# Kernel optimization log

Hardware: AMD Instinct MI355X
Metric: run time of the kernel (lower is better)

Reference implementation:

```python
import jax, jax.numpy as jnp
import numpy as np

NUM_NODES = 100000
EMBED_DIM = 128
COMP_DIM = 64
T = 8
NSUB = 50000


def layer_norm(x, g, b, eps=1e-5):
    mu = jnp.mean(x, axis=-1, keepdims=True)
    var = jnp.mean((x - mu) ** 2, axis=-1, keepdims=True)
    return (x - mu) * jax.lax.rsqrt(var + eps) * g + b


def setup_inputs() -> dict:
    key = jax.random.key(0)
    ks = jax.random.split(key, 12)
    D, C = EMBED_DIM, COMP_DIM
    s = lambda n: 1.0 / np.sqrt(n)
    return {
        "x": jax.random.normal(ks[0], (T * NSUB, D), dtype=jnp.float32),
        "indices": jax.random.randint(ks[1], (T, NSUB), 0, NUM_NODES, dtype=jnp.int64),
        "bd": jax.random.normal(ks[2], (NUM_NODES, D), dtype=jnp.float32),
        "ln_d_g": jnp.ones((D,), jnp.float32), "ln_d_b": jnp.zeros((D,), jnp.float32),
        "Wd1": jax.random.normal(ks[3], (D, 2 * D), jnp.float32) * s(D),
        "bd1": jnp.zeros((2 * D,), jnp.float32),
        "Wd2": jax.random.normal(ks[4], (2 * D, C), jnp.float32) * s(2 * D),
        "bd2": jnp.zeros((C,), jnp.float32),
        "ln_u_g": jnp.ones((C,), jnp.float32), "ln_u_b": jnp.zeros((C,), jnp.float32),
        "Wu1": jax.random.normal(ks[5], (C, 2 * C), jnp.float32) * s(C),
        "bu1": jnp.zeros((2 * C,), jnp.float32),
        "Wu2": jax.random.normal(ks[6], (2 * C, D), jnp.float32) * s(2 * C),
        "bu2": jnp.zeros((D,), jnp.float32),
    }


def reference(x, indices, bd, ln_d_g, ln_d_b, Wd1, bd1, Wd2, bd2,
              ln_u_g, ln_u_b, Wu1, bu1, Wu2, bu2):
    # _to_entire: per-timestep scatter-add of subnode feats into full node table
    x3 = x.reshape(T, NSUB, EMBED_DIM)  # [T, Nsub, D]
    scattered = jax.vmap(
        lambda xt, it: jax.ops.segment_sum(xt, it, num_segments=NUM_NODES)
    )(x3, indices)  # [T, num_nodes, D]
    inp = scattered + bd[None]  # ta + bd (use_bd=True)
    h = layer_norm(inp, ln_d_g, ln_d_b)
    # mlp_d: Linear -> GELU -> Dropout(eval=identity) -> Linear
    h = jax.nn.gelu(h @ Wd1 + bd1, approximate=False) @ Wd2 + bd2  # [T, num_nodes, C]
    # _from_entire: gather activated rows per timestep, then LN + mlp_u
    gathered = jax.vmap(lambda ht, it: ht[it])(h, indices)  # [T, Nsub, C]
    g = gathered.reshape(T * NSUB, COMP_DIM)
    u = layer_norm(g, ln_u_g, ln_u_b)
    out = jax.nn.gelu(u @ Wu1 + bu1, approximate=False) @ Wu2 + bu2  # [T*Nsub, D]
    return out
```

## Files before the change

### kernel.cpp

```cpp
#include <hip/hip_runtime.h>
#include <math.h>

#define NN 100000
#define DD 128
#define CC 64
#define TT 8
#define NS 50000
#define G8 8
#define MAXS2 196
#define BCAP 16

typedef __attribute__((ext_vector_type(4))) float f32x4;
typedef __attribute__((ext_vector_type(8))) short bf16x8;

__device__ __forceinline__ short f2bf(float f) {
    union { float f; unsigned u; } v; v.f = f;
    unsigned r = v.u + 0x7fffu + ((v.u >> 16) & 1u);
    return (short)(r >> 16);
}
__device__ __forceinline__ float gelu(float x) {
    float t = x + 0.044715f * x * x * x;
    return x / (1.0f + __expf(-1.5957691216f * t));
}

__global__ void prep_all(const float* __restrict__ Wd1, const float* __restrict__ Wd2,
                         const float* __restrict__ Wu1, const float* __restrict__ Wu2,
                         short* __restrict__ pW1, short* __restrict__ pW2,
                         short* __restrict__ pW3, short* __restrict__ pW4) {
    int b = blockIdx.x;
    const float* W; short* dst; int KSTEPS, total, N, s0;
    if (b < 16)      { W = Wd1; dst = pW1; KSTEPS = 4; total = 4096; N = 256; s0 = b * 256; }
    else if (b < 24) { W = Wd2; dst = pW2; KSTEPS = 8; total = 2048; N = 64;  s0 = (b - 16) * 256; }
    else if (b < 28) { W = Wu1; dst = pW3; KSTEPS = 2; total = 1024; N = 128; s0 = (b - 24) * 256; }
    else             { W = Wu2; dst = pW4; KSTEPS = 4; total = 2048; N = 128; s0 = (b - 28) * 256; }
    int s = s0 + threadIdx.x;
    if (s >= total) return;
    int lane = s & 63;
    int ks = (s >> 6) % KSTEPS;
    int n = s / (64 * KSTEPS);
    int kb = ks * 32 + (lane >> 4) * 8;
    int col = n * 16 + (lane & 15);
    bf16x8 o;
    #pragma unroll
    for (int j = 0; j < 8; ++j) o[j] = f2bf(W[(size_t)(kb + j) * N + col]);
    *(bf16x8*)(dst + (size_t)s * 8) = o;
}

__global__ void flagfill_kernel(const int* __restrict__ idx, int* __restrict__ pernode,
                                int* __restrict__ bucket) {
    int i = blockIdx.x * 256 + threadIdx.x;
    if (i >= G8 * NS) return;
    int g = i / NS, s = i - g * NS;
    int node = idx[i];
    int p = atomicAdd(&pernode[node * 8 + g], 1);
    if (p < BCAP) bucket[((size_t)node * 8 + g) * BCAP + p] = s;
}

__global__ void compact_kernel(const int* __restrict__ pernode,
                               int* __restrict__ lists, int* __restrict__ cnts) {
    int g = blockIdx.y;
    int node = blockIdx.x * 256 + threadIdx.x;
    bool active = (node < NN) && (pernode[node * 8 + g] > 0);
    unsigned long long m = __ballot(active);
    int lane = threadIdx.x & 63;
    int rank = __popcll(m & ((1ull << lane) - 1ull));
    int nact = __popcll(m);
    int lbase = 0;
    if (lane == 0 && nact > 0) lbase = atomicAdd(&cnts[g], nact);
    lbase = __shfl(lbase, 0);
    if (active) lists[(size_t)g * NS + lbase + rank] = node;
}

__global__ __launch_bounds__(1024, 4) void fused_kernel(
    const float* __restrict__ x, const float* __restrict__ bd,
    const float* __restrict__ lndg, const float* __restrict__ lndb,
    const short* __restrict__ pW1, const short* __restrict__ pW2,
    const short* __restrict__ pW3, const short* __restrict__ pW4,
    const float* __restrict__ bd1, const float* __restrict__ bd2,
    const float* __restrict__ lnug, const float* __restrict__ lnub,
    const float* __restrict__ bu1, const float* __restrict__ bu2,
    const int* __restrict__ lists, const int* __restrict__ cnts,
    const int* __restrict__ pernode, const int* __restrict__ bucket,
    float* __restrict__ out) {
    __shared__ short sW1[4096 * 8];
    __shared__ short sW2[2048 * 8];
    __shared__ short sW4[2048 * 8];
    __shared__ short sBuf[16][1024];

    const int tid = threadIdx.x;
    for (int s = tid; s < 4096; s += 1024)
        *(bf16x8*)(sW1 + s * 8) = *(const bf16x8*)(pW1 + (size_t)s * 8);
    for (int s = tid; s < 2048; s += 1024)
        *(bf16x8*)(sW2 + s * 8) = *(const bf16x8*)(pW2 + (size_t)s * 8);
    for (int s = tid; s < 2048; s += 1024)
        *(bf16x8*)(sW4 + s * 8) = *(const bf16x8*)(pW4 + (size_t)s * 8);
    __syncthreads();

    const int wave = tid >> 6, lane = tid & 63;
    short* myb = sBuf[wave];
    const int arow = lane & 15;
    const int kgrp = lane >> 4;

    for (int w = blockIdx.x; w < G8 * MAXS2; w += gridDim.x) {
        const int g = w % G8;
        const int strip = w / G8;
        const int nrows = cnts[g];
        if (strip * 256 >= nrows) continue;
        const int* list = lists + (size_t)g * NS;
        const float* x_g = x + (size_t)g * NS * DD;
        float* out_g = out + (size_t)g * NS * DD;
        const int row0 = strip * 256 + wave * 16;

        const int gi = row0 + arow;
        const int node = list[gi < nrows ? gi : nrows - 1];
        const int c = pernode[node * 8 + g];
        const size_t bbase = ((size_t)node * 8 + g) * BCAP;
        const int4 p4 = *(const int4*)(bucket + bbase);
        float v[32];
        {
            const float* bp = bd + (size_t)node * DD + kgrp * 8;
            #pragma unroll
            for (int ks = 0; ks < 4; ++ks) {
                float4 b0 = *(const float4*)(bp + ks * 32);
                float4 b1 = *(const float4*)(bp + ks * 32 + 4);
                v[ks*8+0]=b0.x; v[ks*8+1]=b0.y; v[ks*8+2]=b0.z; v[ks*8+3]=b0.w;
                v[ks*8+4]=b1.x; v[ks*8+5]=b1.y; v[ks*8+6]=b1.z; v[ks*8+7]=b1.w;
            }
        }
        {
            const int i1 = (c > 1) ? p4.y : p4.x;
            const float m1 = (c > 1) ? 1.f : 0.f;
            const float* xp0 = x_g + (size_t)p4.x * DD + kgrp * 8;
            const float* xp1 = x_g + (size_t)i1 * DD + kgrp * 8;
            float4 A0[8], A1[8];
            #pragma unroll
            for (int q = 0; q < 8; ++q) A0[q] = *(const float4*)(xp0 + (q >> 1) * 32 + (q & 1) * 4);
            #pragma unroll
            for (int q = 0; q < 8; ++q) A1[q] = *(const float4*)(xp1 + (q >> 1) * 32 + (q & 1) * 4);
            #pragma unroll
            for (int q = 0; q < 8; ++q) {
                v[q*4+0] += A0[q].x; v[q*4+1] += A0[q].y; v[q*4+2] += A0[q].z; v[q*4+3] += A0[q].w;
                v[q*4+0] = fmaf(m1, A1[q].x, v[q*4+0]);
                v[q*4+1] = fmaf(m1, A1[q].y, v[q*4+1]);
                v[q*4+2] = fmaf(m1, A1[q].z, v[q*4+2]);
                v[q*4+3] = fmaf(m1, A1[q].w, v[q*4+3]);
            }
            if (__any(c > 2)) {
                const int i2 = (c > 2) ? p4.z : p4.x;
                const int i3 = (c > 3) ? p4.w : p4.x;
                const float m2 = (c > 2) ? 1.f : 0.f;
                const float m3 = (c > 3) ? 1.f : 0.f;
                const float* xp2 = x_g + (size_t)i2 * DD + kgrp * 8;
                const float* xp3 = x_g + (size_t)i3 * DD + kgrp * 8;
                #pragma unroll
                for (int q = 0; q < 8; ++q) A0[q] = *(const float4*)(xp2 + (q >> 1) * 32 + (q & 1) * 4);
                #pragma unroll
                for (int q = 0; q < 8; ++q) A1[q] = *(const float4*)(xp3 + (q >> 1) * 32 + (q & 1) * 4);
                #pragma unroll
                for (int q = 0; q < 8; ++q) {
                    v[q*4+0] = fmaf(m2, A0[q].x, v[q*4+0]);
                    v[q*4+1] = fmaf(m2, A0[q].y, v[q*4+1]);
                    v[q*4+2] = fmaf(m2, A0[q].z, v[q*4+2]);
                    v[q*4+3] = fmaf(m2, A0[q].w, v[q*4+3]);
                    v[q*4+0] = fmaf(m3, A1[q].x, v[q*4+0]);
                    v[q*4+1] = fmaf(m3, A1[q].y, v[q*4+1]);
                    v[q*4+2] = fmaf(m3, A1[q].z, v[q*4+2]);
                    v[q*4+3] = fmaf(m3, A1[q].w, v[q*4+3]);
                }
                int j = 4;
                while (__any(j < c) && j < BCAP) {
                    const int pj = (j < c) ? bucket[bbase + j] : p4.x;
                    const float mj = (j < c) ? 1.f : 0.f;
                    const float* xpj = x_g + (size_t)pj * DD + kgrp * 8;
                    #pragma unroll
                    for (int q = 0; q < 8; ++q) A0[q] = *(const float4*)(xpj + (q >> 1) * 32 + (q & 1) * 4);
                    #pragma unroll
                    for (int q = 0; q < 8; ++q) {
                        v[q*4+0] = fmaf(mj, A0[q].x, v[q*4+0]);
                        v[q*4+1] = fmaf(mj, A0[q].y, v[q*4+1]);
                        v[q*4+2] = fmaf(mj, A0[q].z, v[q*4+2]);
                        v[q*4+3] = fmaf(mj, A0[q].w, v[q*4+3]);
                    }
                    ++j;
                }
            }
        }
        float s1 = 0.f;
        #pragma unroll
        for (int j = 0; j < 32; ++j) s1 += v[j];
        s1 += __shfl_xor(s1, 16); s1 += __shfl_xor(s1, 32);
        float mu = s1 * 0.0078125f;
        float s2 = 0.f;
        #pragma unroll
        for (int j = 0; j < 32; ++j) { float d = v[j] - mu; s2 += d * d; }
        s2 += __shfl_xor(s2, 16); s2 += __shfl_xor(s2, 32);
        float rs = rsqrtf(s2 * 0.0078125f + 1e-5f);
        bf16x8 afr[4];
        {
            const float* gp = lndg + kgrp * 8;
            const float* bbp = lndb + kgrp * 8;
            #pragma unroll
            for (int ks = 0; ks < 4; ++ks) {
                float4 g0 = *(const float4*)(gp + ks * 32);
                float4 g1 = *(const float4*)(gp + ks * 32 + 4);
                float4 c0 = *(const float4*)(bbp + ks * 32);
                float4 c1 = *(const float4*)(bbp + ks * 32 + 4);
                afr[ks][0] = f2bf((v[ks*8+0]-mu)*rs*g0.x + c0.x);
                afr[ks][1] = f2bf((v[ks*8+1]-mu)*rs*g0.y + c0.y);
                afr[ks][2] = f2bf((v[ks*8+2]-mu)*rs*g0.z + c0.z);
                afr[ks][3] = f2bf((v[ks*8+3]-mu)*rs*g0.w + c0.w);
                afr[ks][4] = f2bf((v[ks*8+4]-mu)*rs*g1.x + c1.x);
                afr[ks][5] = f2bf((v[ks*8+5]-mu)*rs*g1.y + c1.y);
                afr[ks][6] = f2bf((v[ks*8+6]-mu)*rs*g1.z + c1.z);
                afr[ks][7] = f2bf((v[ks*8+7]-mu)*rs*g1.w + c1.w);
            }
        }
        f32x4 acc2[4];
        #pragma unroll
        for (int n = 0; n < 4; ++n) acc2[n] = (f32x4){0.f, 0.f, 0.f, 0.f};
        for (int ks2 = 0; ks2 < 8; ++ks2) {
            f32x4 a1[2];
            a1[0] = (f32x4){0.f, 0.f, 0.f, 0.f};
            a1[1] = (f32x4){0.f, 0.f, 0.f, 0.f};
            #pragma unroll
            for (int ks1 = 0; ks1 < 4; ++ks1) {
                #pragma unroll
                for (int p = 0; p < 2; ++p) {
                    bf16x8 bf = *(const bf16x8*)(sW1 + (size_t)((((2*ks2+p) << 2) | ks1) * 64 + lane) * 8);
                    a1[p] = __builtin_amdgcn_mfma_f32_16x16x32_bf16(afr[ks1], bf, a1[p], 0, 0, 0);
                }
            }
            #pragma unroll
            for (int p = 0; p < 2; ++p) {
                float bias = bd1[(2*ks2+p) * 16 + arow];
                #pragma unroll
                for (int rr = 0; rr < 4; ++rr) {
                    float vv = gelu(a1[p][rr] + bias);
                    int row = kgrp * 4 + rr;
                    int byte = row * 64 + (((p * 16 + arow) * 2) ^ ((row & 3) << 4));
                    myb[byte >> 1] = f2bf(vv);
                }
            }
            bf16x8 af2 = *(const bf16x8*)(myb + ((arow * 64 + ((kgrp * 16) ^ ((arow & 3) << 4))) >> 1));
            #pragma unroll
            for (int n2 = 0; n2 < 4; ++n2) {
                bf16x8 bf = *(const bf16x8*)(sW2 + (size_t)(((n2 << 3) | ks2) * 64 + lane) * 8);
                acc2[n2] = __builtin_amdgcn_mfma_f32_16x16x32_bf16(af2, bf, acc2[n2], 0, 0, 0);
            }
        }
        float hv[4][4];
        #pragma unroll
        for (int n2 = 0; n2 < 4; ++n2)
            #pragma unroll
            for (int rr = 0; rr < 4; ++rr)
                hv[n2][rr] = acc2[n2][rr] + bd2[n2 * 16 + arow];
        float mu_u[4], rs_u[4];
        #pragma unroll
        for (int rr = 0; rr < 4; ++rr) {
            float sr = hv[0][rr] + hv[1][rr] + hv[2][rr] + hv[3][rr];
            sr += __shfl_xor(sr, 1); sr += __shfl_xor(sr, 2);
            sr += __shfl_xor(sr, 4); sr += __shfl_xor(sr, 8);
            mu_u[rr] = sr * 0.015625f;
            float sq = 0.f;
            #pragma unroll
            for (int n2 = 0; n2 < 4; ++n2) { float d = hv[n2][rr] - mu_u[rr]; sq += d * d; }
            sq += __shfl_xor(sq, 1); sq += __shfl_xor(sq, 2);
            sq += __shfl_xor(sq, 4); sq += __shfl_xor(sq, 8);
            rs_u[rr] = rsqrtf(sq * 0.015625f + 1e-5f);
        }
        #pragma unroll
        for (int n2 = 0; n2 < 4; ++n2) {
            int cidx = n2 * 16 + arow;
            float gg = lnug[cidx], bb = lnub[cidx];
            #pragma unroll
            for (int rr = 0; rr < 4; ++rr) {
                float nv = (hv[n2][rr] - mu_u[rr]) * rs_u[rr] * gg + bb;
                int row = kgrp * 4 + rr;
                int byte = row * 128 + ((cidx * 2) ^ ((row & 7) << 4));
                myb[byte >> 1] = f2bf(nv);
            }
        }
        bf16x8 af3[2];
        #pragma unroll
        for (int ks3 = 0; ks3 < 2; ++ks3)
            af3[ks3] = *(const bf16x8*)(myb + ((arow * 128 + ((ks3 * 64 + kgrp * 16) ^ ((arow & 7) << 4))) >> 1));
        f32x4 acc4[8];
        #pragma unroll
        for (int n = 0; n < 8; ++n) acc4[n] = (f32x4){0.f, 0.f, 0.f, 0.f};
        #pragma unroll
        for (int half = 0; half < 2; ++half) {
            f32x4 a3[4];
            #pragma unroll
            for (int n = 0; n < 4; ++n) a3[n] = (f32x4){0.f, 0.f, 0.f, 0.f};
            #pragma unroll
            for (int ks3 = 0; ks3 < 2; ++ks3) {
                #pragma unroll
                for (int n3h = 0; n3h < 4; ++n3h) {
                    int n3 = half * 4 + n3h;
                    bf16x8 bf = *(const bf16x8*)(pW3 + (size_t)(((n3 << 1) | ks3) * 64 + lane) * 8);
                    a3[n3h] = __builtin_amdgcn_mfma_f32_16x16x32_bf16(af3[ks3], bf, a3[n3h], 0, 0, 0);
                }
            }
            #pragma unroll
            for (int n3h = 0; n3h < 4; ++n3h) {
                float bias = bu1[(half * 4 + n3h) * 16 + arow];
                #pragma unroll
                for (int rr = 0; rr < 4; ++rr) {
                    float vv = gelu(a3[n3h][rr] + bias);
                    int row = kgrp * 4 + rr;
                    int byte = row * 128 + (((n3h * 16 + arow) * 2) ^ ((row & 7) << 4));
                    myb[byte >> 1] = f2bf(vv);
                }
            }
            #pragma unroll
            for (int k4 = 0; k4 < 2; ++k4) {
                bf16x8 afu = *(const bf16x8*)(myb + ((arow * 128 + ((k4 * 64 + kgrp * 16) ^ ((arow & 7) << 4))) >> 1));
                #pragma unroll
                for (int n4 = 0; n4 < 8; ++n4) {
                    bf16x8 bf = *(const bf16x8*)(sW4 + (size_t)(((n4 << 2) | (half * 2 + k4)) * 64 + lane) * 8);
                    acc4[n4] = __builtin_amdgcn_mfma_f32_16x16x32_bf16(afu, bf, acc4[n4], 0, 0, 0);
                }
            }
        }
        #pragma unroll
        for (int rr = 0; rr < 4; ++rr) {
            int gi2 = row0 + kgrp * 4 + rr;
            if (gi2 >= nrows) continue;
            int nd = list[gi2];
            int c2 = pernode[nd * 8 + g];
            const size_t bb2 = ((size_t)nd * 8 + g) * BCAP;
            const int4 q4 = *(const int4*)(bucket + bb2);
            float vals[8];
            #pragma unroll
            for (int n4 = 0; n4 < 8; ++n4) vals[n4] = acc4[n4][rr] + bu2[n4 * 16 + arow];
            {
                float* op = out_g + (size_t)q4.x * DD + arow;
                #pragma unroll
                for (int n4 = 0; n4 < 8; ++n4) op[n4 * 16] = vals[n4];
            }
            if (1 < c2) {
                float* op = out_g + (size_t)q4.y * DD + arow;
                #pragma unroll
                for (int n4 = 0; n4 < 8; ++n4) op[n4 * 16] = vals[n4];
            }
            if (2 < c2) {
                float* op = out_g + (size_t)q4.z * DD + arow;
                #pragma unroll
                for (int n4 = 0; n4 < 8; ++n4) op[n4 * 16] = vals[n4];
            }
            if (3 < c2) {
                float* op = out_g + (size_t)q4.w * DD + arow;
                #pragma unroll
                for (int n4 = 0; n4 < 8; ++n4) op[n4 * 16] = vals[n4];
            }
            int j = 4;
            while (__any(j < c2) && j < BCAP) {
                if (j < c2) {
                    int s = bucket[bb2 + j];
                    float* op = out_g + (size_t)s * DD + arow;
                    #pragma unroll
                    for (int n4 = 0; n4 < 8; ++n4) op[n4 * 16] = vals[n4];
                }
                ++j;
            }
        }
    }
}

extern "C" void kernel_launch(void* const* d_in, const int* in_sizes, int n_in,
                              void* d_out, int out_size, void* d_ws, size_t ws_size,
                              hipStream_t stream) {
    const float* x       = (const float*)d_in[0];
    const int*   indices = (const int*)d_in[1];
    const float* bd      = (const float*)d_in[2];
    const float* ln_d_g  = (const float*)d_in[3];
    const float* ln_d_b  = (const float*)d_in[4];
    const float* Wd1     = (const float*)d_in[5];
    const float* bd1     = (const float*)d_in[6];
    const float* Wd2     = (const float*)d_in[7];
    const float* bd2     = (const float*)d_in[8];
    const float* ln_u_g  = (const float*)d_in[9];
    const float* ln_u_b  = (const float*)d_in[10];
    const float* Wu1     = (const float*)d_in[11];
    const float* bu1     = (const float*)d_in[12];
    const float* Wu2     = (const float*)d_in[13];
    const float* bu2     = (const float*)d_in[14];
    float* out = (float*)d_out;

    char* ws = (char*)d_ws;
    size_t o = 0;
    auto alloc_b = [&](size_t bytes) { char* p = ws + o; o = (o + bytes + 255) & ~(size_t)255; return p; };
    int*   pernode  = (int*)alloc_b((size_t)NN * 8 * 4);
    int*   cnts     = (int*)alloc_b(8 * 4);
    size_t zero_bytes = (size_t)((char*)cnts - (char*)pernode) + 256;
    int*   bucket   = (int*)alloc_b((size_t)NN * 8 * BCAP * 4);
    int*   lists    = (int*)alloc_b((size_t)8 * NS * 4);
    short* pW1      = (short*)alloc_b((size_t)4096 * 16);
    short* pW2      = (short*)alloc_b((size_t)2048 * 16);
    short* pW3      = (short*)alloc_b((size_t)1024 * 16);
    short* pW4      = (short*)alloc_b((size_t)2048 * 16);

    hipMemsetAsync(pernode, 0, zero_bytes, stream);

    prep_all<<<36, 256, 0, stream>>>(Wd1, Wd2, Wu1, Wu2, pW1, pW2, pW3, pW4);
    flagfill_kernel<<<(G8 * NS + 255) / 256, 256, 0, stream>>>(indices, pernode, bucket);
    compact_kernel<<<dim3((NN + 255) / 256, G8), 256, 0, stream>>>(pernode, lists, cnts);
    fused_kernel<<<256, 1024, 0, stream>>>(x, bd, ln_d_g, ln_d_b, pW1, pW2, pW3, pW4,
                                           bd1, bd2, ln_u_g, ln_u_b, bu1, bu2,
                                           lists, cnts, pernode, bucket, out);
}
```

Baseline: 468.1 us.

## Prefetch next strip's node metadata and pack bucket indices as 16-bit

Bucket slot indices are stored as 16-bit values, which halves the bucket table footprint and lets a single int4 load return eight source indices instead of four. The fused loop now software-pipelines the list, count and bucket loads for the next work item while the current MLP runs. The aggregation is unrolled up to eight sources with masked FMAs, and LayerNorm outputs are packed to bf16 with the hardware v_cvt_pk_bf16_f32 instruction. The memset now also zeroes the lists region, and the prefetch uses extra registers, which may reduce occupancy.

```diff
diff --git a/kernel.cpp b/kernel.cpp
--- a/kernel.cpp
+++ b/kernel.cpp
@@ -8,15 +8,21 @@
 #define NS 50000
 #define G8 8
 #define MAXS2 196
-#define BCAP 16
+#define TOTW (G8 * MAXS2)
 
 typedef __attribute__((ext_vector_type(4))) float f32x4;
 typedef __attribute__((ext_vector_type(8))) short bf16x8;
+typedef unsigned short ushort_t;
 
 __device__ __forceinline__ short f2bf(float f) {
     union { float f; unsigned u; } v; v.f = f;
     unsigned r = v.u + 0x7fffu + ((v.u >> 16) & 1u);
     return (short)(r >> 16);
+}
+__device__ __forceinline__ unsigned pk_bf16(float lo, float hi) {
+    unsigned r;
+    asm("v_cvt_pk_bf16_f32 %0, %1, %2" : "=v"(r) : "v"(lo), "v"(hi));
+    return r;
 }
 __device__ __forceinline__ float gelu(float x) {
     float t = x + 0.044715f * x * x * x;
@@ -47,13 +53,13 @@
 }
 
 __global__ void flagfill_kernel(const int* __restrict__ idx, int* __restrict__ pernode,
-                                int* __restrict__ bucket) {
+                                ushort_t* __restrict__ bucket) {
     int i = blockIdx.x * 256 + threadIdx.x;
     if (i >= G8 * NS) return;
     int g = i / NS, s = i - g * NS;
     int node = idx[i];
     int p = atomicAdd(&pernode[node * 8 + g], 1);
-    if (p < BCAP) bucket[((size_t)node * 8 + g) * BCAP + p] = s;
+    if (p < 16) bucket[((size_t)node * 8 + g) * 16 + p] = (ushort_t)s;
 }
 
 __global__ void compact_kernel(const int* __restrict__ pernode,
@@ -80,7 +86,7 @@
     const float* __restrict__ lnug, const float* __restrict__ lnub,
     const float* __restrict__ bu1, const float* __restrict__ bu2,
     const int* __restrict__ lists, const int* __restrict__ cnts,
-    const int* __restrict__ pernode, const int* __restrict__ bucket,
+    const int* __restrict__ pernode, const ushort_t* __restrict__ bucket,
     float* __restrict__ out) {
     __shared__ short sW1[4096 * 8];
     __shared__ short sW2[2048 * 8];
@@ -101,269 +107,345 @@
     const int arow = lane & 15;
     const int kgrp = lane >> 4;
 
-    for (int w = blockIdx.x; w < G8 * MAXS2; w += gridDim.x) {
-        const int g = w % G8;
-        const int strip = w / G8;
+    int w = blockIdx.x;
+    int node_c = 0, c_c = 0;
+    int4 p8_c = {0, 0, 0, 0};
+    {
+        int g0 = w & 7, strip0 = w >> 3;
+        int gi0 = strip0 * 256 + wave * 16 + arow;
+        int li0 = gi0 < NS ? gi0 : NS - 1;
+        node_c = lists[(size_t)g0 * NS + li0];
+        c_c = pernode[node_c * 8 + g0];
+        p8_c = *(const int4*)(bucket + ((size_t)node_c * 8 + g0) * 16);
+    }
+
+    for (; w < TOTW; w += gridDim.x) {
+        const int g = w & 7, strip = w >> 3;
         const int nrows = cnts[g];
-        if (strip * 256 >= nrows) continue;
-        const int* list = lists + (size_t)g * NS;
+        const int row0 = strip * 256 + wave * 16;
         const float* x_g = x + (size_t)g * NS * DD;
         float* out_g = out + (size_t)g * NS * DD;
-        const int row0 = strip * 256 + wave * 16;
-
-        const int gi = row0 + arow;
-        const int node = list[gi < nrows ? gi : nrows - 1];
-        const int c = pernode[node * 8 + g];
-        const size_t bbase = ((size_t)node * 8 + g) * BCAP;
-        const int4 p4 = *(const int4*)(bucket + bbase);
-        float v[32];
-        {
-            const float* bp = bd + (size_t)node * DD + kgrp * 8;
-            #pragma unroll
-            for (int ks = 0; ks < 4; ++ks) {
-                float4 b0 = *(const float4*)(bp + ks * 32);
-                float4 b1 = *(const float4*)(bp + ks * 32 + 4);
-                v[ks*8+0]=b0.x; v[ks*8+1]=b0.y; v[ks*8+2]=b0.z; v[ks*8+3]=b0.w;
-                v[ks*8+4]=b1.x; v[ks*8+5]=b1.y; v[ks*8+6]=b1.z; v[ks*8+7]=b1.w;
-            }
-        }
-        {
-            const int i1 = (c > 1) ? p4.y : p4.x;
-            const float m1 = (c > 1) ? 1.f : 0.f;
-            const float* xp0 = x_g + (size_t)p4.x * DD + kgrp * 8;
-            const float* xp1 = x_g + (size_t)i1 * DD + kgrp * 8;
-            float4 A0[8], A1[8];
-            #pragma unroll
-            for (int q = 0; q < 8; ++q) A0[q] = *(const float4*)(xp0 + (q >> 1) * 32 + (q & 1) * 4);
-            #pragma unroll
-            for (int q = 0; q < 8; ++q) A1[q] = *(const float4*)(xp1 + (q >> 1) * 32 + (q & 1) * 4);
-            #pragma unroll
-            for (int q = 0; q < 8; ++q) {
-                v[q*4+0] += A0[q].x; v[q*4+1] += A0[q].y; v[q*4+2] += A0[q].z; v[q*4+3] += A0[q].w;
-                v[q*4+0] = fmaf(m1, A1[q].x, v[q*4+0]);
-                v[q*4+1] = fmaf(m1, A1[q].y, v[q*4+1]);
-                v[q*4+2] = fmaf(m1, A1[q].z, v[q*4+2]);
-                v[q*4+3] = fmaf(m1, A1[q].w, v[q*4+3]);
+
+        const int wn = w + gridDim.x;
+        const bool hn = wn < TOTW;
+        const int gn = hn ? (wn & 7) : 0;
+        const int stripn = hn ? (wn >> 3) : 0;
+        int gin = stripn * 256 + wave * 16 + arow;
+        int lin = gin < NS ? gin : NS - 1;
+        const int node_n = lists[(size_t)gn * NS + lin];
+        int c_n;
+        int4 p8_n;
+
+        if (strip * 256 < nrows) {
+            const int c = c_c;
+            const int pr0 = p8_c.x & 0xffff, pr1 = ((unsigned)p8_c.x) >> 16;
+            const int pr2 = p8_c.y & 0xffff, pr3 = ((unsigned)p8_c.y) >> 16;
+            float v[32];
+            {
+                const float* bp = bd + (size_t)node_c * DD + kgrp * 8;
+                const float* xq0 = x_g + (size_t)pr0 * DD + kgrp * 8;
+                const float* xq1 = x_g + (size_t)((c > 1) ? pr1 : pr0) * DD + kgrp * 8;
+                const float m1 = (c > 1) ? 1.f : 0.f;
+                #pragma unroll
+                for (int ks = 0; ks < 4; ++ks) {
+                    float4 b0 = *(const float4*)(bp + ks * 32);
+                    float4 b1 = *(const float4*)(bp + ks * 32 + 4);
+                    float4 a0 = *(const float4*)(xq0 + ks * 32);
+                    float4 a1 = *(const float4*)(xq0 + ks * 32 + 4);
+                    float4 d0 = *(const float4*)(xq1 + ks * 32);
+                    float4 d1 = *(const float4*)(xq1 + ks * 32 + 4);
+                    v[ks*8+0] = fmaf(m1, d0.x, b0.x + a0.x);
+                    v[ks*8+1] = fmaf(m1, d0.y, b0.y + a0.y);
+                    v[ks*8+2] = fmaf(m1, d0.z, b0.z + a0.z);
+                    v[ks*8+3] = fmaf(m1, d0.w, b0.w + a0.w);
+                    v[ks*8+4] = fmaf(m1, d1.x, b1.x + a1.x);
+                    v[ks*8+5] = fmaf(m1, d1.y, b1.y + a1.y);
+                    v[ks*8+6] = fmaf(m1, d1.z, b1.z + a1.z);
+                    v[ks*8+7] = fmaf(m1, d1.w, b1.w + a1.w);
+                }
             }
             if (__any(c > 2)) {
-                const int i2 = (c > 2) ? p4.z : p4.x;
-                const int i3 = (c > 3) ? p4.w : p4.x;
+                const float* xq2 = x_g + (size_t)((c > 2) ? pr2 : pr0) * DD + kgrp * 8;
+                const float* xq3 = x_g + (size_t)((c > 3) ? pr3 : pr0) * DD + kgrp * 8;
                 const float m2 = (c > 2) ? 1.f : 0.f;
                 const float m3 = (c > 3) ? 1.f : 0.f;
-                const float* xp2 = x_g + (size_t)i2 * DD + kgrp * 8;
-                const float* xp3 = x_g + (size_t)i3 * DD + kgrp * 8;
-                #pragma unroll
-                for (int q = 0; q < 8; ++q) A0[q] = *(const float4*)(xp2 + (q >> 1) * 32 + (q & 1) * 4);
-                #pragma unroll
-                for (int q = 0; q < 8; ++q) A1[q] = *(const float4*)(xp3 + (q >> 1) * 32 + (q & 1) * 4);
-                #pragma unroll
-                for (int q = 0; q < 8; ++q) {
-                    v[q*4+0] = fmaf(m2, A0[q].x, v[q*4+0]);
-                    v[q*4+1] = fmaf(m2, A0[q].y, v[q*4+1]);
-                    v[q*4+2] = fmaf(m2, A0[q].z, v[q*4+2]);
-                    v[q*4+3] = fmaf(m2, A0[q].w, v[q*4+3]);
-                    v[q*4+0] = fmaf(m3, A1[q].x, v[q*4+0]);
-                    v[q*4+1] = fmaf(m3, A1[q].y, v[q*4+1]);
-                    v[q*4+2] = fmaf(m3, A1[q].z, v[q*4+2]);
-                    v[q*4+3] = fmaf(m3, A1[q].w, v[q*4+3]);
-                }
-                int j = 4;
-                while (__any(j < c) && j < BCAP) {
-                    const int pj = (j < c) ? bucket[bbase + j] : p4.x;
+                #pragma unroll
+                for (int ks = 0; ks < 4; ++ks) {
+                    float4 a0 = *(const float4*)(xq2 + ks * 32);
+                    float4 a1 = *(const float4*)(xq2 + ks * 32 + 4);
+                    float4 d0 = *(const float4*)(xq3 + ks * 32);
+                    float4 d1 = *(const float4*)(xq3 + ks * 32 + 4);
+                    v[ks*8+0] = fmaf(m3, d0.x, fmaf(m2, a0.x, v[ks*8+0]));
+                    v[ks*8+1] = fmaf(m3, d0.y, fmaf(m2, a0.y, v[ks*8+1]));
+                    v[ks*8+2] = fmaf(m3, d0.z, fmaf(m2, a0.z, v[ks*8+2]));
+                    v[ks*8+3] = fmaf(m3, d0.w, fmaf(m2, a0.w, v[ks*8+3]));
+                    v[ks*8+4] = fmaf(m3, d1.x, fmaf(m2, a1.x, v[ks*8+4]));
+                    v[ks*8+5] = fmaf(m3, d1.y, fmaf(m2, a1.y, v[ks*8+5]));
+                    v[ks*8+6] = fmaf(m3, d1.z, fmaf(m2, a1.z, v[ks*8+6]));
+                    v[ks*8+7] = fmaf(m3, d1.w, fmaf(m2, a1.w, v[ks*8+7]));
+                }
+            }
+            if (__any(c > 4)) {
+                const int pr4 = p8_c.z & 0xffff, pr5 = ((unsigned)p8_c.z) >> 16;
+                const int pr6 = p8_c.w & 0xffff, pr7 = ((unsigned)p8_c.w) >> 16;
+                const float* xq4 = x_g + (size_t)((c > 4) ? pr4 : pr0) * DD + kgrp * 8;
+                const float* xq5 = x_g + (size_t)((c > 5) ? pr5 : pr0) * DD + kgrp * 8;
+                const float* xq6 = x_g + (size_t)((c > 6) ? pr6 : pr0) * DD + kgrp * 8;
+                const float* xq7 = x_g + (size_t)((c > 7) ? pr7 : pr0) * DD + kgrp * 8;
+                const float m4 = (c > 4) ? 1.f : 0.f;
+                const float m5 = (c > 5) ? 1.f : 0.f;
+                const float m6 = (c > 6) ? 1.f : 0.f;
+                const float m7 = (c > 7) ? 1.f : 0.f;
+                #pragma unroll
+                for (int ks = 0; ks < 4; ++ks) {
+                    float4 a0 = *(const float4*)(xq4 + ks * 32);
+                    float4 a1 = *(const float4*)(xq4 + ks * 32 + 4);
+                    float4 d0 = *(const float4*)(xq5 + ks * 32);
+                    float4 d1 = *(const float4*)(xq5 + ks * 32 + 4);
+                    float4 e0 = *(const float4*)(xq6 + ks * 32);
+                    float4 e1 = *(const float4*)(xq6 + ks * 32 + 4);
+                    float4 f0 = *(const float4*)(xq7 + ks * 32);
+                    float4 f1 = *(const float4*)(xq7 + ks * 32 + 4);
+                    #pragma unroll
+                    for (int q = 0; q < 4; ++q) {
+                        float av = (&a0.x)[q], dv = (&d0.x)[q], ev = (&e0.x)[q], fv = (&f0.x)[q];
+                        v[ks*8+q] = fmaf(m7, fv, fmaf(m6, ev, fmaf(m5, dv, fmaf(m4, av, v[ks*8+q]))));
+                        float av1 = (&a1.x)[q], dv1 = (&d1.x)[q], ev1 = (&e1.x)[q], fv1 = (&f1.x)[q];
+                        v[ks*8+4+q] = fmaf(m7, fv1, fmaf(m6, ev1, fmaf(m5, dv1, fmaf(m4, av1, v[ks*8+4+q]))));
+                    }
+                }
+            }
+            if (__any(c > 8)) {
+                const ushort_t* bt = bucket + ((size_t)node_c * 8 + g) * 16;
+                for (int j = 8; j < 16; ++j) {
+                    const int pj = (j < c) ? bt[j] : pr0;
                     const float mj = (j < c) ? 1.f : 0.f;
-                    const float* xpj = x_g + (size_t)pj * DD + kgrp * 8;
-                    #pragma unroll
-                    for (int q = 0; q < 8; ++q) A0[q] = *(const float4*)(xpj + (q >> 1) * 32 + (q & 1) * 4);
-                    #pragma unroll
-                    for (int q = 0; q < 8; ++q) {
-                        v[q*4+0] = fmaf(mj, A0[q].x, v[q*4+0]);
-                        v[q*4+1] = fmaf(mj, A0[q].y, v[q*4+1]);
-                        v[q*4+2] = fmaf(mj, A0[q].z, v[q*4+2]);
-                        v[q*4+3] = fmaf(mj, A0[q].w, v[q*4+3]);
-                    }
-                    ++j;
-                }
-            }
+                    const float* xq = x_g + (size_t)pj * DD + kgrp * 8;
+                    #pragma unroll
+                    for (int ks = 0; ks < 4; ++ks) {
+                        float4 a0 = *(const float4*)(xq + ks * 32);
+                        float4 a1 = *(const float4*)(xq + ks * 32 + 4);
+                        v[ks*8+0] = fmaf(mj, a0.x, v[ks*8+0]);
+                        v[ks*8+1] = fmaf(mj, a0.y, v[ks*8+1]);
+                        v[ks*8+2] = fmaf(mj, a0.z, v[ks*8+2]);
+                        v[ks*8+3] = fmaf(mj, a0.w, v[ks*8+3]);
+                        v[ks*8+4] = fmaf(mj, a1.x, v[ks*8+4]);
+                        v[ks*8+5] = fmaf(mj, a1.y, v[ks*8+5]);
+                        v[ks*8+6] = fmaf(mj, a1.z, v[ks*8+6]);
+                        v[ks*8+7] = fmaf(mj, a1.w, v[ks*8+7]);
+                    }
+                }
+            }
+            float s1 = 0.f;
+            #pragma unroll
+            for (int j = 0; j < 32; ++j) s1 += v[j];
+            s1 += __shfl_xor(s1, 16); s1 += __shfl_xor(s1, 32);
+            float mu = s1 * 0.0078125f;
+            float s2 = 0.f;
+            #pragma unroll
+            for (int j = 0; j < 32; ++j) { float d = v[j] - mu; s2 += d * d; }
+            s2 += __shfl_xor(s2, 16); s2 += __shfl_xor(s2, 32);
+            float rs = rsqrtf(s2 * 0.0078125f + 1e-5f);
+            union U8 { bf16x8 v8; unsigned u[4]; };
+            bf16x8 afr[4];
+            {
+                const float* gp = lndg + kgrp * 8;
+                const float* bbp = lndb + kgrp * 8;
+                #pragma unroll
+                for (int ks = 0; ks < 4; ++ks) {
+                    float4 g0 = *(const float4*)(gp + ks * 32);
+                    float4 g1 = *(const float4*)(gp + ks * 32 + 4);
+                    float4 c0 = *(const float4*)(bbp + ks * 32);
+                    float4 c1 = *(const float4*)(bbp + ks * 32 + 4);
+                    U8 t;
+                    t.u[0] = pk_bf16((v[ks*8+0]-mu)*rs*g0.x + c0.x, (v[ks*8+1]-mu)*rs*g0.y + c0.y);
+                    t.u[1] = pk_bf16((v[ks*8+2]-mu)*rs*g0.z + c0.z, (v[ks*8+3]-mu)*rs*g0.w + c0.w);
+                    t.u[2] = pk_bf16((v[ks*8+4]-mu)*rs*g1.x + c1.x, (v[ks*8+5]-mu)*rs*g1.y + c1.y);
+                    t.u[3] = pk_bf16((v[ks*8+6]-mu)*rs*g1.z + c1.z, (v[ks*8+7]-mu)*rs*g1.w + c1.w);
+                    afr[ks] = t.v8;
+                }
+            }
+            f32x4 acc2[4];
+            #pragma unroll
+            for (int n = 0; n < 4; ++n) acc2[n] = (f32x4){0.f, 0.f, 0.f, 0.f};
+            for (int ks2 = 0; ks2 < 8; ++ks2) {
+                f32x4 a1v[2];
+                a1v[0] = (f32x4){0.f, 0.f, 0.f, 0.f};
+                a1v[1] = (f32x4){0.f, 0.f, 0.f, 0.f};
+                #pragma unroll
+                for (int ks1 = 0; ks1 < 4; ++ks1) {
+                    #pragma unroll
+                    for (int p = 0; p < 2; ++p) {
+                        bf16x8 bf = *(const bf16x8*)(sW1 + (size_t)((((2*ks2+p) << 2) | ks1) * 64 + lane) * 8);
+                        a1v[p] = __builtin_amdgcn_mfma_f32_16x16x32_bf16(afr[ks1], bf, a1v[p], 0, 0, 0);
+                    }
+                }
+                #pragma unroll
+                for (int p = 0; p < 2; ++p) {
+                    float bias = bd1[(2*ks2+p) * 16 + arow];
+                    #pragma unroll
+                    for (int rr = 0; rr < 4; ++rr) {
+                        float vv = gelu(a1v[p][rr] + bias);
+                        int row = kgrp * 4 + rr;
+                        int byte = row * 64 + (((p * 16 + arow) * 2) ^ ((row & 3) << 4));
+                        myb[byte >> 1] = f2bf(vv);
+                    }
+                }
+                bf16x8 af2 = *(const bf16x8*)(myb + ((arow * 64 + ((kgrp * 16) ^ ((arow & 3) << 4))) >> 1));
+                #pragma unroll
+                for (int n2 = 0; n2 < 4; ++n2) {
+                    bf16x8 bf = *(const bf16x8*)(sW2 + (size_t)(((n2 << 3) | ks2) * 64 + lane) * 8);
+                    acc2[n2] = __builtin_amdgcn_mfma_f32_16x16x32_bf16(af2, bf, acc2[n2], 0, 0, 0);
+                }
+            }
+            c_n = pernode[node_n * 8 + gn];
+            p8_n = *(const int4*)(bucket + ((size_t)node_n * 8 + gn) * 16);
+            float hv[4][4];
+            #pragma unroll
+            for (int n2 = 0; n2 < 4; ++n2)
+                #pragma unroll
+                for (int rr = 0; rr < 4; ++rr)
+                    hv[n2][rr] = acc2[n2][rr] + bd2[n2 * 16 + arow];
+            float mu_u[4], rs_u[4];
+            #pragma unroll
+            for (int rr = 0; rr < 4; ++rr) {
+                float sr = hv[0][rr] + hv[1][rr] + hv[2][rr] + hv[3][rr];
+                sr += __shfl_xor(sr, 1); sr += __shfl_xor(sr, 2);
+                sr += __shfl_xor(sr, 4); sr += __shfl_xor(sr, 8);
+                mu_u[rr] = sr * 0.015625f;
+                float sq = 0.f;
+                #pragma unroll
+                for (int n2 = 0; n2 < 4; ++n2) { float d = hv[n2][rr] - mu_u[rr]; sq += d * d; }
+                sq += __shfl_xor(sq, 1); sq += __shfl_xor(sq, 2);
+                sq += __shfl_xor(sq, 4); sq += __shfl_xor(sq, 8);
+                rs_u[rr] = rsqrtf(sq * 0.015625f + 1e-5f);
+            }
+            #pragma unroll
+            for (int n2 = 0; n2 < 4; ++n2) {
+                int cidx = n2 * 16 + arow;
+                float gg = lnug[cidx], bb = lnub[cidx];
+                #pragma unroll
+                for (int rr = 0; rr < 4; ++rr) {
+                    float nv = (hv[n2][rr] - mu_u[rr]) * rs_u[rr] * gg + bb;
+                    int row = kgrp * 4 + rr;
+                    int byte = row * 128 + ((cidx * 2) ^ ((row & 7) << 4));
+                    myb[byte >> 1] = f2bf(nv);
+                }
+            }
+            bf16x8 af3[2];
+            #pragma unroll
+            for (int ks3 = 0; ks3 < 2; ++ks3)
+                af3[ks3] = *(const bf16x8*)(myb + ((arow * 128 + ((ks3 * 64 + kgrp * 16) ^ ((arow & 7) << 4))) >> 1));
+            f32x4 acc4[8];
+            #pragma unroll
+            for (int n = 0; n < 8; ++n) acc4[n] = (f32x4){0.f, 0.f, 0.f, 0.f};
+            #pragma unroll
+            for (int half = 0; half < 2; ++half) {
+                f32x4 a3[4];
+                #pragma unroll
+                for (int n = 0; n < 4; ++n) a3[n] = (f32x4){0.f, 0.f, 0.f, 0.f};
+                #pragma unroll
+                for (int ks3 = 0; ks3 < 2; ++ks3) {
+                    #pragma unroll
+                    for (int n3h = 0; n3h < 4; ++n3h) {
+                        int n3 = half * 4 + n3h;
+                        bf16x8 bf = *(const bf16x8*)(pW3 + (size_t)(((n3 << 1) | ks3) * 64 + lane) * 8);
+                        a3[n3h] = __builtin_amdgcn_mfma_f32_16x16x32_bf16(af3[ks3], bf, a3[n3h], 0, 0, 0);
+                    }
+                }
+                #pragma unroll
+                for (int n3h = 0; n3h < 4; ++n3h) {
+                    float bias = bu1[(half * 4 + n3h) * 16 + arow];
+                    #pragma unroll
+                    for (int rr = 0; rr < 4; ++rr) {
+                        float vv = gelu(a3[n3h][rr] + bias);
+                        int row = kgrp * 4 + rr;
+                        int byte = row * 128 + (((n3h * 16 + arow) * 2) ^ ((row & 7) << 4));
+                        myb[byte >> 1] = f2bf(vv);
+                    }
+                }
+                #pragma unroll
+                for (int k4 = 0; k4 < 2; ++k4) {
+                    bf16x8 afu = *(const bf16x8*)(myb + ((arow * 128 + ((k4 * 64 + kgrp * 16) ^ ((arow & 7) << 4))) >> 1));
+                    #pragma unroll
+                    for (int n4 = 0; n4 < 8; ++n4) {
+                        bf16x8 bf = *(const bf16x8*)(sW4 + (size_t)(((n4 << 2) | (half * 2 + k4)) * 64 + lane) * 8);
+                        acc4[n4] = __builtin_amdgcn_mfma_f32_16x16x32_bf16(afu, bf, acc4[n4], 0, 0, 0);
+                    }
+                }
+            }
+            #pragma unroll
+            for (int rr = 0; rr < 4; ++rr) {
+                const int src = kgrp * 4 + rr;
+                const int c2  = __shfl(c_c, src);
+                const unsigned w0 = (unsigned)__shfl(p8_c.x, src);
+                const unsigned w1 = (unsigned)__shfl(p8_c.y, src);
+                const unsigned w2 = (unsigned)__shfl(p8_c.z, src);
+                const unsigned w3 = (unsigned)__shfl(p8_c.w, src);
+                const int nd  = __shfl(node_c, src);
+                const int gi2 = row0 + kgrp * 4 + rr;
+                if (gi2 >= nrows) continue;
+                float vals[8];
+                #pragma unroll
+                for (int n4 = 0; n4 < 8; ++n4) vals[n4] = acc4[n4][rr] + bu2[n4 * 16 + arow];
+                {
+                    float* op = out_g + (size_t)(w0 & 0xffff) * DD + arow;
+                    #pragma unroll
+                    for (int n4 = 0; n4 < 8; ++n4) op[n4 * 16] = vals[n4];
+                }
+                if (c2 > 1) {
+                    float* op = out_g + (size_t)(w0 >> 16) * DD + arow;
+                    #pragma unroll
+                    for (int n4 = 0; n4 < 8; ++n4) op[n4 * 16] = vals[n4];
+                }
+                if (c2 > 2) {
+                    float* op = out_g + (size_t)(w1 & 0xffff) * DD + arow;
+                    #pragma unroll
+                    for (int n4 = 0; n4 < 8; ++n4) op[n4 * 16] = vals[n4];
+                }
+                if (c2 > 3) {
+                    float* op = out_g + (size_t)(w1 >> 16) * DD + arow;
+                    #pragma unroll
+                    for (int n4 = 0; n4 < 8; ++n4) op[n4 * 16] = vals[n4];
+                }
+                if (__any(c2 > 4)) {
+                    if (c2 > 4) {
+                        float* op = out_g + (size_t)(w2 & 0xffff) * DD + arow;
+                        #pragma unroll
+                        for (int n4 = 0; n4 < 8; ++n4) op[n4 * 16] = vals[n4];
+                    }
+                    if (c2 > 5) {
+                        float* op = out_g + (size_t)(w2 >> 16) * DD + arow;
+                        #pragma unroll
+                        for (int n4 = 0; n4 < 8; ++n4) op[n4 * 16] = vals[n4];
+                    }
+                    if (c2 > 6) {
+                        float* op = out_g + (size_t)(w3 & 0xffff) * DD + arow;
+                        #pragma unroll
+                        for (int n4 = 0; n4 < 8; ++n4) op[n4 * 16] = vals[n4];
+                    }
+                    if (c2 > 7) {
+                        float* op = out_g + (size_t)(w3 >> 16) * DD + arow;
+                        #pragma unroll
+                        for (int n4 = 0; n4 < 8; ++n4) op[n4 * 16] = vals[n4];
+                    }
+                }
+                if (__any(c2 > 8)) {
+                    const ushort_t* bt = bucket + ((size_t)nd * 8 + g) * 16;
+                    for (int j = 8; j < 16; ++j) {
+                        if (j < c2) {
+                            float* op = out_g + (size_t)bt[j] * DD + arow;
+                            #pragma unroll
+                            for (int n4 = 0; n4 < 8; ++n4) op[n4 * 16] = vals[n4];
+                        }
+                    }
+                }
+            }
+        } else {
+            c_n = pernode[node_n * 8 + gn];
+            p8_n = *(const int4*)(bucket + ((size_t)node_n * 8 + gn) * 16);
         }
-        float s1 = 0.f;
-        #pragma unroll
-        for (int j = 0; j < 32; ++j) s1 += v[j];
-        s1 += __shfl_xor(s1, 16); s1 += __shfl_xor(s1, 32);
-        float mu = s1 * 0.0078125f;
-        float s2 = 0.f;
-        #pragma unroll
-        for (int j = 0; j < 32; ++j) { float d = v[j] - mu; s2 += d * d; }
-        s2 += __shfl_xor(s2, 16); s2 += __shfl_xor(s2, 32);
-        float rs = rsqrtf(s2 * 0.0078125f + 1e-5f);
-        bf16x8 afr[4];
-        {
-            const float* gp = lndg + kgrp * 8;
-            const float* bbp = lndb + kgrp * 8;
-            #pragma unroll
-            for (int ks = 0; ks < 4; ++ks) {
-                float4 g0 = *(const float4*)(gp + ks * 32);
-                float4 g1 = *(const float4*)(gp + ks * 32 + 4);
-                float4 c0 = *(const float4*)(bbp + ks * 32);
-                float4 c1 = *(const float4*)(bbp + ks * 32 + 4);
-                afr[ks][0] = f2bf((v[ks*8+0]-mu)*rs*g0.x + c0.x);
-                afr[ks][1] = f2bf((v[ks*8+1]-mu)*rs*g0.y + c0.y);
-                afr[ks][2] = f2bf((v[ks*8+2]-mu)*rs*g0.z + c0.z);
-                afr[ks][3] = f2bf((v[ks*8+3]-mu)*rs*g0.w + c0.w);
-                afr[ks][4] = f2bf((v[ks*8+4]-mu)*rs*g1.x + c1.x);
-                afr[ks][5] = f2bf((v[ks*8+5]-mu)*rs*g1.y + c1.y);
-                afr[ks][6] = f2bf((v[ks*8+6]-mu)*rs*g1.z + c1.z);
-                afr[ks][7] = f2bf((v[ks*8+7]-mu)*rs*g1.w + c1.w);
-            }
-        }
-        f32x4 acc2[4];
-        #pragma unroll
-        for (int n = 0; n < 4; ++n) acc2[n] = (f32x4){0.f, 0.f, 0.f, 0.f};
-        for (int ks2 = 0; ks2 < 8; ++ks2) {
-            f32x4 a1[2];
-            a1[0] = (f32x4){0.f, 0.f, 0.f, 0.f};
-            a1[1] = (f32x4){0.f, 0.f, 0.f, 0.f};
-            #pragma unroll
-            for (int ks1 = 0; ks1 < 4; ++ks1) {
-                #pragma unroll
-                for (int p = 0; p < 2; ++p) {
-                    bf16x8 bf = *(const bf16x8*)(sW1 + (size_t)((((2*ks2+p) << 2) | ks1) * 64 + lane) * 8);
-                    a1[p] = __builtin_amdgcn_mfma_f32_16x16x32_bf16(afr[ks1], bf, a1[p], 0, 0, 0);
-                }
-            }
-            #pragma unroll
-            for (int p = 0; p < 2; ++p) {
-                float bias = bd1[(2*ks2+p) * 16 + arow];
-                #pragma unroll
-                for (int rr = 0; rr < 4; ++rr) {
-                    float vv = gelu(a1[p][rr] + bias);
-                    int row = kgrp * 4 + rr;
-                    int byte = row * 64 + (((p * 16 + arow) * 2) ^ ((row & 3) << 4));
-                    myb[byte >> 1] = f2bf(vv);
-                }
-            }
-            bf16x8 af2 = *(const bf16x8*)(myb + ((arow * 64 + ((kgrp * 16) ^ ((arow & 3) << 4))) >> 1));
-            #pragma unroll
-            for (int n2 = 0; n2 < 4; ++n2) {
-                bf16x8 bf = *(const bf16x8*)(sW2 + (size_t)(((n2 << 3) | ks2) * 64 + lane) * 8);
-                acc2[n2] = __builtin_amdgcn_mfma_f32_16x16x32_bf16(af2, bf, acc2[n2], 0, 0, 0);
-            }
-        }
-        float hv[4][4];
-        #pragma unroll
-        for (int n2 = 0; n2 < 4; ++n2)
-            #pragma unroll
-            for (int rr = 0; rr < 4; ++rr)
-                hv[n2][rr] = acc2[n2][rr] + bd2[n2 * 16 + arow];
-        float mu_u[4], rs_u[4];
-        #pragma unroll
-        for (int rr = 0; rr < 4; ++rr) {
-            float sr = hv[0][rr] + hv[1][rr] + hv[2][rr] + hv[3][rr];
-            sr += __shfl_xor(sr, 1); sr += __shfl_xor(sr, 2);
-            sr += __shfl_xor(sr, 4); sr += __shfl_xor(sr, 8);
-            mu_u[rr] = sr * 0.015625f;
-            float sq = 0.f;
-            #pragma unroll
-            for (int n2 = 0; n2 < 4; ++n2) { float d = hv[n2][rr] - mu_u[rr]; sq += d * d; }
-            sq += __shfl_xor(sq, 1); sq += __shfl_xor(sq, 2);
-            sq += __shfl_xor(sq, 4); sq += __shfl_xor(sq, 8);
-            rs_u[rr] = rsqrtf(sq * 0.015625f + 1e-5f);
-        }
-        #pragma unroll
-        for (int n2 = 0; n2 < 4; ++n2) {
-            int cidx = n2 * 16 + arow;
-            float gg = lnug[cidx], bb = lnub[cidx];
-            #pragma unroll
-            for (int rr = 0; rr < 4; ++rr) {
-                float nv = (hv[n2][rr] - mu_u[rr]) * rs_u[rr] * gg + bb;
-                int row = kgrp * 4 + rr;
-                int byte = row * 128 + ((cidx * 2) ^ ((row & 7) << 4));
-                myb[byte >> 1] = f2bf(nv);
-            }
-        }
-        bf16x8 af3[2];
-        #pragma unroll
-        for (int ks3 = 0; ks3 < 2; ++ks3)
-            af3[ks3] = *(const bf16x8*)(myb + ((arow * 128 + ((ks3 * 64 + kgrp * 16) ^ ((arow & 7) << 4))) >> 1));
-        f32x4 acc4[8];
-        #pragma unroll
-        for (int n = 0; n < 8; ++n) acc4[n] = (f32x4){0.f, 0.f, 0.f, 0.f};
-        #pragma unroll
-        for (int half = 0; half < 2; ++half) {
-            f32x4 a3[4];
-            #pragma unroll
-            for (int n = 0; n < 4; ++n) a3[n] = (f32x4){0.f, 0.f, 0.f, 0.f};
-            #pragma unroll
-            for (int ks3 = 0; ks3 < 2; ++ks3) {
-                #pragma unroll
-                for (int n3h = 0; n3h < 4; ++n3h) {
-                    int n3 = half * 4 + n3h;
-                    bf16x8 bf = *(const bf16x8*)(pW3 + (size_t)(((n3 << 1) | ks3) * 64 + lane) * 8);
-                    a3[n3h] = __builtin_amdgcn_mfma_f32_16x16x32_bf16(af3[ks3], bf, a3[n3h], 0, 0, 0);
-                }
-            }
-            #pragma unroll
-            for (int n3h = 0; n3h < 4; ++n3h) {
-                float bias = bu1[(half * 4 + n3h) * 16 + arow];
-                #pragma unroll
-                for (int rr = 0; rr < 4; ++rr) {
-                    float vv = gelu(a3[n3h][rr] + bias);
-                    int row = kgrp * 4 + rr;
-                    int byte = row * 128 + (((n3h * 16 + arow) * 2) ^ ((row & 7) << 4));
-                    myb[byte >> 1] = f2bf(vv);
-                }
-            }
-            #pragma unroll
-            for (int k4 = 0; k4 < 2; ++k4) {
-                bf16x8 afu = *(const bf16x8*)(myb + ((arow * 128 + ((k4 * 64 + kgrp * 16) ^ ((arow & 7) << 4))) >> 1));
-                #pragma unroll
-                for (int n4 = 0; n4 < 8; ++n4) {
-                    bf16x8 bf = *(const bf16x8*)(sW4 + (size_t)(((n4 << 2) | (half * 2 + k4)) * 64 + lane) * 8);
-                    acc4[n4] = __builtin_amdgcn_mfma_f32_16x16x32_bf16(afu, bf, acc4[n4], 0, 0, 0);
-                }
-            }
-        }
-        #pragma unroll
-        for (int rr = 0; rr < 4; ++rr) {
-            int gi2 = row0 + kgrp * 4 + rr;
-            if (gi2 >= nrows) continue;
-            int nd = list[gi2];
-            int c2 = pernode[nd * 8 + g];
-            const size_t bb2 = ((size_t)nd * 8 + g) * BCAP;
-            const int4 q4 = *(const int4*)(bucket + bb2);
-            float vals[8];
-            #pragma unroll
-            for (int n4 = 0; n4 < 8; ++n4) vals[n4] = acc4[n4][rr] + bu2[n4 * 16 + arow];
-            {
-                float* op = out_g + (size_t)q4.x * DD + arow;
-                #pragma unroll
-                for (int n4 = 0; n4 < 8; ++n4) op[n4 * 16] = vals[n4];
-            }
-            if (1 < c2) {
-                float* op = out_g + (size_t)q4.y * DD + arow;
-                #pragma unroll
-                for (int n4 = 0; n4 < 8; ++n4) op[n4 * 16] = vals[n4];
-            }
-            if (2 < c2) {
-                float* op = out_g + (size_t)q4.z * DD + arow;
-                #pragma unroll
-                for (int n4 = 0; n4 < 8; ++n4) op[n4 * 16] = vals[n4];
-            }
-            if (3 < c2) {
-                float* op = out_g + (size_t)q4.w * DD + arow;
-                #pragma unroll
-                for (int n4 = 0; n4 < 8; ++n4) op[n4 * 16] = vals[n4];
-            }
-            int j = 4;
-            while (__any(j < c2) && j < BCAP) {
-                if (j < c2) {
-                    int s = bucket[bb2 + j];
-                    float* op = out_g + (size_t)s * DD + arow;
-                    #pragma unroll
-                    for (int n4 = 0; n4 < 8; ++n4) op[n4 * 16] = vals[n4];
-                }
-                ++j;
-            }
-        }
+        node_c = node_n; c_c = c_n; p8_c = p8_n;
     }
 }
 
@@ -390,15 +472,15 @@
     char* ws = (char*)d_ws;
     size_t o = 0;
     auto alloc_b = [&](size_t bytes) { char* p = ws + o; o = (o + bytes + 255) & ~(size_t)255; return p; };
-    int*   pernode  = (int*)alloc_b((size_t)NN * 8 * 4);
-    int*   cnts     = (int*)alloc_b(8 * 4);
-    size_t zero_bytes = (size_t)((char*)cnts - (char*)pernode) + 256;
-    int*   bucket   = (int*)alloc_b((size_t)NN * 8 * BCAP * 4);
-    int*   lists    = (int*)alloc_b((size_t)8 * NS * 4);
-    short* pW1      = (short*)alloc_b((size_t)4096 * 16);
-    short* pW2      = (short*)alloc_b((size_t)2048 * 16);
-    short* pW3      = (short*)alloc_b((size_t)1024 * 16);
-    short* pW4      = (short*)alloc_b((size_t)2048 * 16);
+    int*      pernode = (int*)alloc_b((size_t)NN * 8 * 4);
+    int*      cnts    = (int*)alloc_b(8 * 4);
+    int*      lists   = (int*)alloc_b((size_t)8 * NS * 4);
+    size_t zero_bytes = (size_t)((char*)lists - (char*)pernode) + (size_t)8 * NS * 4;
+    ushort_t* bucket  = (ushort_t*)alloc_b((size_t)NN * 8 * 16 * 2);
+    short*    pW1     = (short*)alloc_b((size_t)4096 * 16);
+    short*    pW2     = (short*)alloc_b((size_t)2048 * 16);
+    short*    pW3     = (short*)alloc_b((size_t)1024 * 16);
+    short*    pW4     = (short*)alloc_b((size_t)2048 * 16);
 
     hipMemsetAsync(pernode, 0, zero_bytes, stream);
 
```

Measured after the change: 483.0 us. +3.2%, slower.
